# Kernel tuning notes

Hardware: AMD Instinct MI355X
Metric: run time of the kernel (lower is better)

The kernel has to match this reference:

```python
import jax, jax.numpy as jnp
import numpy as np

B, DIN, E, FACTOR, STEPS, NH = 2048, 1024, 1024, 16, 3, 8
DH = E // NH
EPS = 1e-5


def layernorm(x, g, b):
    m = x.mean(-1, keepdims=True)
    v = ((x - m) ** 2).mean(-1, keepdims=True)
    return (x - m) / jnp.sqrt(v + EPS) * g + b


def setup_inputs() -> dict:
    key = jax.random.key(0)
    ks = iter(jax.random.split(key, 32))
    r = lambda shape, s=0.02: jax.random.normal(next(ks), shape, dtype=jnp.float32) * s
    F = E * FACTOR
    return {
        "image_feat": jax.random.normal(next(ks), (B, DIN), dtype=jnp.float32),
        "text_feat": jax.random.normal(next(ks), (B, DIN), dtype=jnp.float32),
        # fusion block
        "fc1_w": r((F, DIN)), "fc1_b": jnp.zeros((F,), jnp.float32),
        "fc2_w": r((F, DIN)), "fc2_b": jnp.zeros((F,), jnp.float32),
        "fc3_w": r((E, F)), "fc3_b": jnp.zeros((E,), jnp.float32),
        "ln_g": jnp.ones((E,), jnp.float32), "ln_b": jnp.zeros((E,), jnp.float32),
        # per-step MHA + FFN + norms, stacked over STEPS
        "Wqkv": r((STEPS, 3 * E, E)), "bqkv": jnp.zeros((STEPS, 3 * E), jnp.float32),
        "Wo": r((STEPS, E, E)), "bo": jnp.zeros((STEPS, E), jnp.float32),
        "W1": r((STEPS, E, E)), "b1": jnp.zeros((STEPS, E), jnp.float32),
        "W2": r((STEPS, E, E)), "b2": jnp.zeros((STEPS, E), jnp.float32),
        "n1_g": jnp.ones((STEPS, E), jnp.float32), "n1_b": jnp.zeros((STEPS, E), jnp.float32),
        "n2_g": jnp.ones((STEPS, E), jnp.float32), "n2_b": jnp.zeros((STEPS, E), jnp.float32),
        # output projection
        "Wout": r((DIN, E)), "bout": jnp.zeros((DIN,), jnp.float32),
    }


def mha_step(q, ctx, Wqkv, bqkv, Wo, bo):
    # q: [B,E] (query len 1), ctx: [B,L,E]
    Wq, Wk, Wv = Wqkv[:E], Wqkv[E:2 * E], Wqkv[2 * E:]
    bq, bk, bv = bqkv[:E], bqkv[E:2 * E], bqkv[2 * E:]
    L = ctx.shape[1]
    qh = (q @ Wq.T + bq).reshape(B, NH, DH)
    kh = (ctx @ Wk.T + bk).reshape(B, L, NH, DH)
    vh = (ctx @ Wv.T + bv).reshape(B, L, NH, DH)
    scores = jnp.einsum("bhd,blhd->bhl", qh, kh) / jnp.sqrt(jnp.float32(DH))
    attn = jax.nn.softmax(scores, axis=-1)
    out = jnp.einsum("bhl,blhd->bhd", attn, vh).reshape(B, E)
    return out @ Wo.T + bo


def reference(image_feat, text_feat, fc1_w, fc1_b, fc2_w, fc2_b, fc3_w, fc3_b,
              ln_g, ln_b, Wqkv, bqkv, Wo, bo, W1, b1, W2, b2,
              n1_g, n1_b, n2_g, n2_b, Wout, bout):
    # fusion block (dropout = identity in eval)
    fused = (image_feat @ fc1_w.T + fc1_b) * (text_feat @ fc2_w.T + fc2_b)
    fused = layernorm(fused @ fc3_w.T + fc3_b, ln_g, ln_b)  # [B,E]
    ctx = fused[:, None, :]  # [B,1,E]
    x = fused
    for i in range(STEPS):
        attn = mha_step(x, ctx, Wqkv[i], bqkv[i], Wo[i], bo[i])
        x = x + layernorm(attn, n1_g[i], n1_b[i])
        ffn = jax.nn.relu(x @ W1[i].T + b1[i]) @ W2[i].T + b2[i]
        x = x + layernorm(ffn, n2_g[i], n2_b[i])
        ctx = jnp.concatenate([ctx, x[:, None, :]], axis=1)
    final_output = x @ Wout.T + bout  # [B,DIN]
    return final_output, ctx
```

## Files before the change

### kernel.cpp

```cpp
#include <hip/hip_runtime.h>

#define TB 256

typedef __attribute__((ext_vector_type(8))) short short8;
typedef __attribute__((ext_vector_type(4))) float f32x4;
typedef unsigned short u16;

constexpr int B_  = 2048;
constexpr int DIN = 1024;
constexpr int E   = 1024;
constexpr int F   = 16384;
constexpr int E3  = 3072;
constexpr int CH  = 4096;

struct Ptr8 { void* p[8]; };

__device__ __forceinline__ u16 f2bf(float f) {
  union { float f; unsigned u; } v; v.f = f;
  unsigned r = v.u + 0x7fffu + ((v.u >> 16) & 1u);
  return (u16)(r >> 16);
}
__device__ __forceinline__ float bf2f(u16 u) {
  union { unsigned u; float f; } v; v.u = ((unsigned)u) << 16;
  return v.f;
}

__device__ __forceinline__ void gload16(const void* g, void* l) {
  __builtin_amdgcn_global_load_lds(
      (const __attribute__((address_space(1))) void*)g,
      (__attribute__((address_space(3))) void*)l, 16, 0, 0);
}

__device__ __forceinline__ void tile_xy(int& tx, int& ty) {
  int gx = gridDim.x;
  int nwg = gx * gridDim.y;
  int wg = blockIdx.y * gx + blockIdx.x;
  if ((nwg & 7) == 0) wg = (wg & 7) * (nwg >> 3) + (wg >> 3);
  tx = wg % gx; ty = wg / gx;
}

__device__ __forceinline__ int swz16(int o) {
  return o ^ (((o >> 7) & 7) << 4);
}

__global__ __launch_bounds__(256) void cvt_kernel(const float* __restrict__ s,
                                                  u16* __restrict__ d, int n) {
  int i = (blockIdx.x * 256 + threadIdx.x) * 4;
  if (i >= n) return;
  float4 v = *(const float4*)&s[i];
  ushort4 o;
  o.x = f2bf(v.x); o.y = f2bf(v.y); o.z = f2bf(v.z); o.w = f2bf(v.w);
  *(ushort4*)&d[i] = o;
}

__global__ __launch_bounds__(256) void fill_kernel(float* p, int n, float v) {
  int i = blockIdx.x * 256 + threadIdx.x;
  if (i < n) p[i] = v;
}

__global__ __launch_bounds__(256) void relu_multi_kernel(
    Ptr8 ys, int ny, const float* __restrict__ bias, u16* __restrict__ out) {
  size_t i = ((size_t)blockIdx.x * 256 + threadIdx.x) * 4;
  int col = (int)(i & 1023);
  float4 b = *(const float4*)&bias[col];
  float a0 = b.x, a1 = b.y, a2 = b.z, a3 = b.w;
  for (int j = 0; j < ny; ++j) {
    float4 z = *(const float4*)&((const float*)ys.p[j])[i];
    a0 += z.x; a1 += z.y; a2 += z.z; a3 += z.w;
  }
  ushort4 o;
  o.x = f2bf(a0 > 0.f ? a0 : 0.f);
  o.y = f2bf(a1 > 0.f ? a1 : 0.f);
  o.z = f2bf(a2 > 0.f ? a2 : 0.f);
  o.w = f2bf(a3 > 0.f ? a3 : 0.f);
  *(ushort4*)&out[i] = o;
}

__global__ __launch_bounds__(256) void combine_out_kernel(
    Ptr8 ys, int ny, const float* __restrict__ bias, float* __restrict__ out) {
  size_t i = ((size_t)blockIdx.x * 256 + threadIdx.x) * 4;
  int col = (int)(i & 1023);
  float4 b = *(const float4*)&bias[col];
  float a0 = b.x, a1 = b.y, a2 = b.z, a3 = b.w;
  for (int j = 0; j < ny; ++j) {
    float4 z = *(const float4*)&((const float*)ys.p[j])[i];
    a0 += z.x; a1 += z.y; a2 += z.z; a3 += z.w;
  }
  out[i] = a0; out[i + 1] = a1; out[i + 2] = a2; out[i + 3] = a3;
}

template <int EPI>
__global__ __launch_bounds__(512, 2) void gemm256(
    const u16* __restrict__ A, int sA,
    const u16* __restrict__ Bw, int sB,
    const float* __restrict__ bias, const u16* __restrict__ gate,
    void* __restrict__ Out, Ptr8 pouts, int ldOut, int ksz) {
  __shared__ __align__(16) char smem[131072];
  const int tid = threadIdx.x, lane = tid & 63, w = tid >> 6;
  const int wm = w >> 2, wn = w & 3;
  int tx, ty; tile_xy(tx, ty);
  const int m0 = tx * 256, n0 = ty * 256;
  const int k0 = blockIdx.z * ksz;
  const int nt = ksz >> 6;
  const int lr = lane & 15;

  f32x4 acc[8][4] = {};

  auto stage = [&](const u16* __restrict__ G, int gs, int gr0, int kk, int tb, int j) {
    int P = j * 8192 + w * 1024 + lane * 16;
    int L = swz16(P);
    int row = L >> 7, colb = L & 127;
    gload16(G + (size_t)(gr0 + row) * gs + kk + (colb >> 1),
            &smem[tb + j * 8192 + w * 1024]);
  };
  auto rdA = [&](int tb, int mf, int kh) -> short8 {
    int Lo = (wm * 128 + mf * 16 + lr) * 128 + kh * 64 + (lane >> 4) * 16;
    return *(const short8*)&smem[tb + swz16(Lo)];
  };
  auto rdB = [&](int tb, int nf, int kh) -> short8 {
    int Lo = (wn * 64 + nf * 16 + lr) * 128 + kh * 64 + (lane >> 4) * 16;
    return *(const short8*)&smem[tb + swz16(Lo)];
  };

#pragma unroll
  for (int j = 0; j < 4; ++j) stage(A, sA, m0, k0, 0, j);
#pragma unroll
  for (int j = 0; j < 4; ++j) stage(Bw, sB, n0, k0, 65536, j);
  asm volatile("s_waitcnt vmcnt(0)" ::: "memory");
  __builtin_amdgcn_sched_barrier(0);
  __builtin_amdgcn_s_barrier();

  int cur = 0;
  for (int t = 0; t < nt; ++t) {
    const int sa = cur * 32768;
    const int sb = 65536 + cur * 32768;
    if (t + 1 < nt) {
      const int sa2 = (cur ^ 1) * 32768;
      const int sb2 = 65536 + (cur ^ 1) * 32768;
#pragma unroll
      for (int j = 0; j < 4; ++j) stage(A, sA, m0, k0 + (t + 1) * 64, sa2, j);
#pragma unroll
      for (int j = 0; j < 4; ++j) stage(Bw, sB, n0, k0 + (t + 1) * 64, sb2, j);
    }
    short8 bfr[4][2], afr[4][2];
#pragma unroll
    for (int nf = 0; nf < 4; ++nf)
#pragma unroll
      for (int kh = 0; kh < 2; ++kh) bfr[nf][kh] = rdB(sb, nf, kh);
#pragma unroll
    for (int mf = 0; mf < 4; ++mf)
#pragma unroll
      for (int kh = 0; kh < 2; ++kh) afr[mf][kh] = rdA(sa, mf, kh);
    __builtin_amdgcn_s_setprio(1);
#pragma unroll
    for (int mf = 0; mf < 4; ++mf)
#pragma unroll
      for (int nf = 0; nf < 4; ++nf)
#pragma unroll
        for (int kh = 0; kh < 2; ++kh)
          acc[mf][nf] = __builtin_amdgcn_mfma_f32_16x16x32_bf16(
              afr[mf][kh], bfr[nf][kh], acc[mf][nf], 0, 0, 0);
    __builtin_amdgcn_s_setprio(0);
#pragma unroll
    for (int mf = 0; mf < 4; ++mf)
#pragma unroll
      for (int kh = 0; kh < 2; ++kh) afr[mf][kh] = rdA(sa, 4 + mf, kh);
    __builtin_amdgcn_s_setprio(1);
#pragma unroll
    for (int mf = 0; mf < 4; ++mf)
#pragma unroll
      for (int nf = 0; nf < 4; ++nf)
#pragma unroll
        for (int kh = 0; kh < 2; ++kh)
          acc[4 + mf][nf] = __builtin_amdgcn_mfma_f32_16x16x32_bf16(
              afr[mf][kh], bfr[nf][kh], acc[4 + mf][nf], 0, 0, 0);
    __builtin_amdgcn_s_setprio(0);
    if (t + 1 < nt) {
      asm volatile("s_waitcnt vmcnt(0)" ::: "memory");
      __builtin_amdgcn_sched_barrier(0);
      __builtin_amdgcn_s_barrier();
    }
    cur ^= 1;
  }

  if (EPI == 0) {
    float* Pf = (float*)pouts.p[blockIdx.z];
    const int rb = (lane >> 4) * 4;
#pragma unroll
    for (int mf = 0; mf < 8; ++mf) {
#pragma unroll
      for (int nf = 0; nf < 4; ++nf) {
        int row0 = m0 + wm * 128 + mf * 16 + rb;
        int col  = n0 + wn * 64 + nf * 16 + lr;
#pragma unroll
        for (int r = 0; r < 4; ++r)
          Pf[(size_t)(row0 + r) * ldOut + col] = acc[mf][nf][r];
      }
    }
  } else {
    __syncthreads();
    char* wbase = smem + w * 16384;
    const int rb = (lane >> 4) * 4;
    const int g4 = lane >> 4;
#pragma unroll
    for (int mf = 0; mf < 8; ++mf) {
      char* wmf = wbase + mf * 2048;
#pragma unroll
      for (int nf = 0; nf < 4; ++nf) {
        float bv = (bias == nullptr) ? 0.f : bias[n0 + wn * 64 + nf * 16 + lr];
        int pb = nf ^ g4;
#pragma unroll
        for (int r = 0; r < 4; ++r)
          *(u16*)&wmf[(rb + r) * 128 + pb * 32 + lr * 2] =
              f2bf(acc[mf][nf][r] + bv);
      }
      asm volatile("s_waitcnt lgkmcnt(0)" ::: "memory");
      __builtin_amdgcn_sched_barrier(0);
      int rrow = lane >> 2, wb = lane & 3;
      int pb2 = wb ^ (rrow >> 2);
      short8 v0 = *(const short8*)&wmf[rrow * 128 + pb2 * 32];
      short8 v1 = *(const short8*)&wmf[rrow * 128 + pb2 * 32 + 16];
      size_t gidx = (size_t)(m0 + wm * 128 + mf * 16 + rrow) * ldOut +
                    (n0 + wn * 64 + wb * 16);
      if (EPI == 4) {
        short8 g0 = *(const short8*)&gate[gidx];
        short8 g1 = *(const short8*)&gate[gidx + 8];
        short8 o0, o1;
#pragma unroll
        for (int j = 0; j < 8; ++j) {
          o0[j] = (short)f2bf(bf2f((u16)v0[j]) * bf2f((u16)g0[j]));
          o1[j] = (short)f2bf(bf2f((u16)v1[j]) * bf2f((u16)g1[j]));
        }
        *(short8*)((u16*)Out + gidx) = o0;
        *(short8*)((u16*)Out + gidx + 8) = o1;
      } else {
        *(short8*)((u16*)Out + gidx) = v0;
        *(short8*)((u16*)Out + gidx + 8) = v1;
      }
    }
  }
}

template <int EPI>
__global__ __launch_bounds__(TB) void gemm_bt(
    const u16* __restrict__ A, int sA,
    const u16* __restrict__ Bw, int sB,
    const float* __restrict__ bias, Ptr8 outs,
    int ldOut, int Kext, int ksz) {
  __shared__ u16 As[128 * 32];
  __shared__ u16 Bs[128 * 32];
  const int tid = threadIdx.x, lane = tid & 63, w = tid >> 6;
  const int wr = w >> 1, wc = w & 1;
  int tx, ty; tile_xy(tx, ty);
  const int m0 = tx * 128, n0 = ty * 128;
  const int k0 = blockIdx.z * ksz;
  const int kend = min(k0 + ksz, Kext);

  f32x4 acc[4][4] = {};
  const int lr = lane & 15, lk = (lane >> 4) * 8;

  for (int kk = k0; kk < kend; kk += 32) {
#pragma unroll
    for (int is = 0; is < 2; ++is) {
      int c = is * 256 + tid;
      int r = c >> 2, kc = (c & 3) << 3;
      size_t lb = (size_t)(is * 256 + w * 64) * 8;
      gload16(A  + (size_t)(m0 + r) * sA + kk + kc, &As[lb]);
      gload16(Bw + (size_t)(n0 + r) * sB + kk + kc, &Bs[lb]);
    }
    __syncthreads();
    short8 af[4], bfv[4];
#pragma unroll
    for (int m = 0; m < 4; ++m)
      af[m] = *(const short8*)&As[(wr * 64 + m * 16 + lr) * 32 + lk];
#pragma unroll
    for (int n = 0; n < 4; ++n)
      bfv[n] = *(const short8*)&Bs[(wc * 64 + n * 16 + lr) * 32 + lk];
#pragma unroll
    for (int m = 0; m < 4; ++m)
#pragma unroll
      for (int n = 0; n < 4; ++n)
        acc[m][n] = __builtin_amdgcn_mfma_f32_16x16x32_bf16(af[m], bfv[n], acc[m][n], 0, 0, 0);
    __syncthreads();
  }

  float* Of = (float*)outs.p[EPI == 0 ? blockIdx.z : 0];
  const int rbase = (lane >> 4) * 4;
#pragma unroll
  for (int m = 0; m < 4; ++m) {
#pragma unroll
    for (int n = 0; n < 4; ++n) {
      int row0 = m0 + wr * 64 + m * 16 + rbase;
      int col  = n0 + wc * 64 + n * 16 + lr;
      float bv = (bias == nullptr) ? 0.f : bias[col];
#pragma unroll
      for (int r = 0; r < 4; ++r) {
        float v = acc[m][n][r] + bv;
        size_t idx = (size_t)(row0 + r) * ldOut + col;
        if (EPI == 0) Of[idx] = v;
        else          ((u16*)Of)[idx] = f2bf(v);
      }
    }
  }
}

template <int EPI>
__global__ __launch_bounds__(TB) void gemm_wf32(
    const u16* __restrict__ A, int sA,
    const float* __restrict__ Bw, int sB,
    const float* __restrict__ bias, void* __restrict__ Out, int ldOut,
    int Kext, int ksz) {
  __shared__ u16 As[128 * 32];
  __shared__ u16 Bs[128 * 32];
  const int tid = threadIdx.x, lane = tid & 63, w = tid >> 6;
  const int wr = w >> 1, wc = w & 1;
  int tx, ty; tile_xy(tx, ty);
  const int m0 = tx * 128, n0 = ty * 128;
  const int k0 = blockIdx.z * ksz;
  const int kend = min(k0 + ksz, Kext);

  f32x4 acc[4][4] = {};
  const int lr = lane & 15, lk = (lane >> 4) * 8;

  for (int kk = k0; kk < kend; kk += 32) {
#pragma unroll
    for (int is = 0; is < 2; ++is) {
      int c = is * 256 + tid;
      int r = c >> 2, kc = (c & 3) << 3;
      gload16(A + (size_t)(m0 + r) * sA + kk + kc,
              &As[(size_t)(is * 256 + w * 64) * 8]);
    }
#pragma unroll
    for (int p = 0; p < 4; ++p) {
      int t = tid + p * 256;
      int r = t >> 3, c4 = (t & 7) << 2;
      float4 v = *(const float4*)&Bw[(size_t)(n0 + r) * sB + kk + c4];
      ushort4 o;
      o.x = f2bf(v.x); o.y = f2bf(v.y); o.z = f2bf(v.z); o.w = f2bf(v.w);
      *(ushort4*)&Bs[r * 32 + c4] = o;
    }
    __syncthreads();
    short8 af[4], bfv[4];
#pragma unroll
    for (int m = 0; m < 4; ++m)
      af[m] = *(const short8*)&As[(wr * 64 + m * 16 + lr) * 32 + lk];
#pragma unroll
    for (int n = 0; n < 4; ++n)
      bfv[n] = *(const short8*)&Bs[(wc * 64 + n * 16 + lr) * 32 + lk];
#pragma unroll
    for (int m = 0; m < 4; ++m)
#pragma unroll
      for (int n = 0; n < 4; ++n)
        acc[m][n] = __builtin_amdgcn_mfma_f32_16x16x32_bf16(af[m], bfv[n], acc[m][n], 0, 0, 0);
    __syncthreads();
  }

  const int rbase = (lane >> 4) * 4;
#pragma unroll
  for (int m = 0; m < 4; ++m) {
#pragma unroll
    for (int n = 0; n < 4; ++n) {
      int row0 = m0 + wr * 64 + m * 16 + rbase;
      int col  = n0 + wc * 64 + n * 16 + lr;
      float bv = (EPI == 3 || bias == nullptr) ? 0.f : bias[col];
#pragma unroll
      for (int r = 0; r < 4; ++r) {
        float v = acc[m][n][r] + bv;
        size_t idx = (size_t)(row0 + r) * ldOut + col;
        if (EPI == 0)      ((float*)Out)[idx] = v;
        else if (EPI == 1) ((u16*)Out)[idx] = f2bf(v);
        else if (EPI == 2) ((u16*)Out)[idx] = f2bf(v > 0.f ? v : 0.f);
        else               atomicAdd((float*)Out + idx, v);
      }
    }
  }
}

__global__ __launch_bounds__(TB) void gemm_dual_wf32(
    const u16* __restrict__ A1, const u16* __restrict__ A2, int sA,
    const float* __restrict__ B1, const float* __restrict__ B2, int sB,
    const float* __restrict__ bias1, const float* __restrict__ bias2,
    u16* __restrict__ Out, int ldOut, int K) {
  __shared__ u16 As1[128 * 32];
  __shared__ u16 As2[128 * 32];
  __shared__ u16 Bs1[128 * 32];
  __shared__ u16 Bs2[128 * 32];
  const int tid = threadIdx.x, lane = tid & 63, w = tid >> 6;
  const int wr = w >> 1, wc = w & 1;
  int tx, ty; tile_xy(tx, ty);
  const int m0 = tx * 128, n0 = ty * 128;

  f32x4 acc1[4][4] = {};
  f32x4 acc2[4][4] = {};
  const int lr = lane & 15, lk = (lane >> 4) * 8;

  for (int kk = 0; kk < K; kk += 32) {
#pragma unroll
    for (int is = 0; is < 2; ++is) {
      int c = is * 256 + tid;
      int r = c >> 2, kc = (c & 3) << 3;
      size_t lb = (size_t)(is * 256 + w * 64) * 8;
      gload16(A1 + (size_t)(m0 + r) * sA + kk + kc, &As1[lb]);
      gload16(A2 + (size_t)(m0 + r) * sA + kk + kc, &As2[lb]);
    }
#pragma unroll
    for (int p = 0; p < 4; ++p) {
      int t = tid + p * 256;
      int r = t >> 3, c4 = (t & 7) << 2;
      float4 v1 = *(const float4*)&B1[(size_t)(n0 + r) * sB + kk + c4];
      float4 v2 = *(const float4*)&B2[(size_t)(n0 + r) * sB + kk + c4];
      ushort4 o1, o2;
      o1.x = f2bf(v1.x); o1.y = f2bf(v1.y); o1.z = f2bf(v1.z); o1.w = f2bf(v1.w);
      o2.x = f2bf(v2.x); o2.y = f2bf(v2.y); o2.z = f2bf(v2.z); o2.w = f2bf(v2.w);
      *(ushort4*)&Bs1[r * 32 + c4] = o1;
      *(ushort4*)&Bs2[r * 32 + c4] = o2;
    }
    __syncthreads();
    short8 a1[4], a2[4], b1v[4], b2v[4];
#pragma unroll
    for (int m = 0; m < 4; ++m) {
      a1[m] = *(const short8*)&As1[(wr * 64 + m * 16 + lr) * 32 + lk];
      a2[m] = *(const short8*)&As2[(wr * 64 + m * 16 + lr) * 32 + lk];
    }
#pragma unroll
    for (int n = 0; n < 4; ++n) {
      b1v[n] = *(const short8*)&Bs1[(wc * 64 + n * 16 + lr) * 32 + lk];
      b2v[n] = *(const short8*)&Bs2[(wc * 64 + n * 16 + lr) * 32 + lk];
    }
#pragma unroll
    for (int m = 0; m < 4; ++m)
#pragma unroll
      for (int n = 0; n < 4; ++n) {
        acc1[m][n] = __builtin_amdgcn_mfma_f32_16x16x32_bf16(a1[m], b1v[n], acc1[m][n], 0, 0, 0);
        acc2[m][n] = __builtin_amdgcn_mfma_f32_16x16x32_bf16(a2[m], b2v[n], acc2[m][n], 0, 0, 0);
      }
    __syncthreads();
  }

  const int rbase = (lane >> 4) * 4;
#pragma unroll
  for (int m = 0; m < 4; ++m) {
#pragma unroll
    for (int n = 0; n < 4; ++n) {
      int row0 = m0 + wr * 64 + m * 16 + rbase;
      int col  = n0 + wc * 64 + n * 16 + lr;
      float bv1 = bias1[col], bv2 = bias2[col];
#pragma unroll
      for (int r = 0; r < 4; ++r) {
        float v = (acc1[m][n][r] + bv1) * (acc2[m][n][r] + bv2);
        Out[(size_t)(row0 + r) * ldOut + col] = f2bf(v);
      }
    }
  }
}

template <int MODE>
__global__ __launch_bounds__(256) void resln_kernel(
    Ptr8 ys, int ny, const float* __restrict__ preb,
    const float* __restrict__ g, const float* __restrict__ bp,
    float* __restrict__ x, u16* __restrict__ xb,
    float* __restrict__ ctxo, int ctxRow) {
  const int r = blockIdx.x, tid = threadIdx.x;
  const size_t base = (size_t)r * 1024 + tid * 4;
  float y[4] = {0.f, 0.f, 0.f, 0.f};
  for (int j = 0; j < ny; ++j) {
    float4 z = *(const float4*)&((const float*)ys.p[j])[base];
    y[0] += z.x; y[1] += z.y; y[2] += z.z; y[3] += z.w;
  }
  if (preb != nullptr) {
    float4 p4 = *(const float4*)&preb[tid * 4];
    y[0] += p4.x; y[1] += p4.y; y[2] += p4.z; y[3] += p4.w;
  }
  float s = y[0] + y[1] + y[2] + y[3];
  float q = y[0] * y[0] + y[1] * y[1] + y[2] * y[2] + y[3] * y[3];
  __shared__ float red[8];
  for (int o = 32; o; o >>= 1) { s += __shfl_xor(s, o); q += __shfl_xor(q, o); }
  int wv = tid >> 6;
  if ((tid & 63) == 0) { red[wv] = s; red[4 + wv] = q; }
  __syncthreads();
  s = red[0] + red[1] + red[2] + red[3];
  q = red[4] + red[5] + red[6] + red[7];
  float mean = s * (1.f / 1024.f);
  float var  = q * (1.f / 1024.f) - mean * mean;
  float rs   = rsqrtf(var + 1e-5f);
  float4 g4 = *(const float4*)&g[tid * 4];
  float4 b4 = *(const float4*)&bp[tid * 4];
  float gg[4] = {g4.x, g4.y, g4.z, g4.w};
  float bb[4] = {b4.x, b4.y, b4.z, b4.w};
  float xv[4];
#pragma unroll
  for (int j = 0; j < 4; ++j) {
    float val = (y[j] - mean) * rs * gg[j] + bb[j];
    xv[j] = (MODE == 0) ? val : x[base + j] + val;
  }
  *(float4*)&x[base] = make_float4(xv[0], xv[1], xv[2], xv[3]);
  ushort4 xo;
  xo.x = f2bf(xv[0]); xo.y = f2bf(xv[1]); xo.z = f2bf(xv[2]); xo.w = f2bf(xv[3]);
  *(ushort4*)&xb[base] = xo;
  if (MODE != 1) {
    size_t cb = ((size_t)r * 4 + ctxRow) * 1024 + tid * 4;
    *(float4*)&ctxo[cb] = make_float4(xv[0], xv[1], xv[2], xv[3]);
  }
}

__global__ __launch_bounds__(64) void attn_kernel(
    const u16* __restrict__ q, int qstride,
    const u16* __restrict__ kv, int kvstride, int voff,
    u16* __restrict__ out, int L) {
  const int b = blockIdx.x >> 3, h = blockIdx.x & 7;
  const int lane = threadIdx.x;
  const size_t qoff = (size_t)b * qstride + h * 128;
  float q0 = bf2f(q[qoff + lane]);
  float q1 = bf2f(q[qoff + 64 + lane]);
  float sc[3];
  for (int l = 0; l < L; ++l) {
    size_t kb = ((size_t)l * B_ + b) * kvstride + h * 128;
    float p = q0 * bf2f(kv[kb + lane]) + q1 * bf2f(kv[kb + 64 + lane]);
    for (int o = 32; o; o >>= 1) p += __shfl_xor(p, o);
    sc[l] = p * 0.08838834764831843f;
  }
  float m = sc[0];
  for (int l = 1; l < L; ++l) m = fmaxf(m, sc[l]);
  float wsum = 0.f, wgt[3];
  for (int l = 0; l < L; ++l) { wgt[l] = expf(sc[l] - m); wsum += wgt[l]; }
  float inv = 1.f / wsum;
  float o0 = 0.f, o1 = 0.f;
  for (int l = 0; l < L; ++l) {
    size_t vb = ((size_t)l * B_ + b) * kvstride + voff + h * 128;
    o0 += wgt[l] * bf2f(kv[vb + lane]);
    o1 += wgt[l] * bf2f(kv[vb + 64 + lane]);
  }
  out[(size_t)b * 1024 + h * 128 + lane]      = f2bf(o0 * inv);
  out[(size_t)b * 1024 + h * 128 + 64 + lane] = f2bf(o1 * inv);
}

extern "C" void kernel_launch(void* const* d_in, const int* in_sizes, int n_in,
                              void* d_out, int out_size, void* d_ws, size_t ws_size,
                              hipStream_t stream) {
  (void)in_sizes; (void)n_in;
  const float* image = (const float*)d_in[0];
  const float* text  = (const float*)d_in[1];
  const float* fc1_w = (const float*)d_in[2];
  const float* fc1_b = (const float*)d_in[3];
  const float* fc2_w = (const float*)d_in[4];
  const float* fc2_b = (const float*)d_in[5];
  const float* fc3_w = (const float*)d_in[6];
  const float* fc3_b = (const float*)d_in[7];
  const float* ln_g  = (const float*)d_in[8];
  const float* ln_b  = (const float*)d_in[9];
  const float* Wqkv  = (const float*)d_in[10];
  const float* bqkv  = (const float*)d_in[11];
  const float* Wo    = (const float*)d_in[12];
  const float* bo    = (const float*)d_in[13];
  const float* W1    = (const float*)d_in[14];
  const float* b1    = (const float*)d_in[15];
  const float* W2    = (const float*)d_in[16];
  const float* b2    = (const float*)d_in[17];
  const float* n1_g  = (const float*)d_in[18];
  const float* n1_b  = (const float*)d_in[19];
  const float* n2_g  = (const float*)d_in[20];
  const float* n2_b  = (const float*)d_in[21];
  const float* WoutW = (const float*)d_in[22];
  const float* boutW = (const float*)d_in[23];

  float* outF   = (float*)d_out;
  float* ctxOut = outF + (size_t)B_ * DIN;
  char* ws = (char*)d_ws;

  auto cvt = [&](const float* s, u16* d, size_t n) {
    cvt_kernel<<<dim3((unsigned)((n + 1023) / 1024)), 256, 0, stream>>>(s, d, (int)n);
  };

  const size_t NEED_A = 232783872;
  if (ws_size >= NEED_A) {
    size_t off = 0;
    auto carve = [&](size_t bytes) -> char* {
      char* p = ws + off; off += (bytes + 255) & ~(size_t)255; return p;
    };
    u16* imgB  = (u16*)carve((size_t)B_ * DIN * 2);
    u16* txtB  = (u16*)carve((size_t)B_ * DIN * 2);
    u16* fc1B  = (u16*)carve((size_t)F * DIN * 2);
    u16* fc2B  = (u16*)carve((size_t)F * DIN * 2);
    u16* fc3B  = (u16*)carve((size_t)E * F * 2);
    u16* WqkvB = (u16*)carve((size_t)3 * E3 * E * 2);
    u16* WoB   = (u16*)carve((size_t)3 * E * E * 2);
    u16* W1B   = (u16*)carve((size_t)3 * E * E * 2);
    u16* W2B   = (u16*)carve((size_t)3 * E * E * 2);
    u16* WoutB = (u16*)carve((size_t)DIN * E * 2);
    char* U    = carve((size_t)B_ * F * 2);
    float* xF  = (float*)carve((size_t)B_ * E * 4);
    float* hF  = (float*)carve((size_t)B_ * E * 4);
    u16* fusedB = (u16*)U;
    u16* kvB    = (u16*)(U);
    u16* qB     = (u16*)(U + 25165824);
    u16* ctxB   = (u16*)(U + 37748736);
    u16* attnB  = (u16*)(U + 37748736 + 16777216);
    u16* h1B    = (u16*)(U + 37748736 + 16777216 + 4194304);
    u16* xbB    = (u16*)(U + 37748736 + 16777216 + 8388608);
    float* PA = (float*)fc1B;
    float* PB = (float*)(fc1B + 4194304);
    float* PC = (float*)(fc1B + 8388608);
    float* PD = (float*)(fc1B + 12582912);
    float* PE = (float*)fc2B;
    float* PF = (float*)(fc2B + 4194304);

    cvt(image, imgB, (size_t)B_ * DIN);
    cvt(text,  txtB, (size_t)B_ * DIN);
    cvt(fc1_w, fc1B, (size_t)F * DIN);
    cvt(fc2_w, fc2B, (size_t)F * DIN);
    cvt(fc3_w, fc3B, (size_t)E * F);
    cvt(Wqkv,  WqkvB, (size_t)3 * E3 * E);
    cvt(Wo,    WoB,   (size_t)3 * E * E);
    cvt(W1,    W1B,   (size_t)3 * E * E);
    cvt(W2,    W2B,   (size_t)3 * E * E);
    cvt(WoutW, WoutB, (size_t)DIN * E);

    Ptr8 dumb{};
    gemm256<1><<<dim3(B_ / 256, F / 256), 512, 0, stream>>>(
        txtB, DIN, fc2B, DIN, fc2_b, nullptr, fusedB, dumb, F, DIN);
    gemm256<4><<<dim3(B_ / 256, F / 256), 512, 0, stream>>>(
        imgB, DIN, fc1B, DIN, fc1_b, fusedB, fusedB, dumb, F, DIN);
    Ptr8 p8f{{xF, hF, PA, PB, PC, PD, PE, PF}};
    gemm256<0><<<dim3(B_ / 256, E / 256, 8), 512, 0, stream>>>(
        fusedB, F, fc3B, F, nullptr, nullptr, nullptr, p8f, E, F / 8);
    resln_kernel<0><<<B_, 256, 0, stream>>>(
        p8f, 8, fc3_b, ln_g, ln_b, xF, ctxB, ctxOut, 0);

    Ptr8 p4{{hF, outF, PA, PB, nullptr, nullptr, nullptr, nullptr}};
    for (int i = 0; i < 3; ++i) {
      int L = i + 1;
      Ptr8 qkv1{{kvB, nullptr, nullptr, nullptr, nullptr, nullptr, nullptr, nullptr}};
      gemm_bt<1><<<dim3(L * B_ / 128, 2 * E / 128), TB, 0, stream>>>(
          ctxB, E, WqkvB + (size_t)i * E3 * E + (size_t)E * E, E,
          bqkv + (size_t)i * E3 + E, qkv1, 2 * E, E, E);
      Ptr8 qkv2{{qB, nullptr, nullptr, nullptr, nullptr, nullptr, nullptr, nullptr}};
      gemm_bt<1><<<dim3(B_ / 128, E / 128), TB, 0, stream>>>(
          ctxB + (size_t)i * B_ * E, E, WqkvB + (size_t)i * E3 * E, E,
          bqkv + (size_t)i * E3, qkv2, E, E, E);
      attn_kernel<<<B_ * 8, 64, 0, stream>>>(qB, E, kvB, 2 * E, E, attnB, L);
      gemm_bt<0><<<dim3(B_ / 128, E / 128, 4), TB, 0, stream>>>(
          attnB, E, WoB + (size_t)i * E * E, E, nullptr, p4, E, E, E / 4);
      resln_kernel<1><<<B_, 256, 0, stream>>>(
          p4, 4, bo + (size_t)i * E, n1_g + (size_t)i * E, n1_b + (size_t)i * E,
          xF, xbB, nullptr, 0);
      gemm_bt<0><<<dim3(B_ / 128, E / 128, 4), TB, 0, stream>>>(
          xbB, E, W1B + (size_t)i * E * E, E, nullptr, p4, E, E, E / 4);
      relu_multi_kernel<<<B_ * E / 1024, 256, 0, stream>>>(
          p4, 4, b1 + (size_t)i * E, h1B);
      gemm_bt<0><<<dim3(B_ / 128, E / 128, 4), TB, 0, stream>>>(
          h1B, E, W2B + (size_t)i * E * E, E, nullptr, p4, E, E, E / 4);
      resln_kernel<2><<<B_, 256, 0, stream>>>(
          p4, 4, b2 + (size_t)i * E, n2_g + (size_t)i * E, n2_b + (size_t)i * E,
          xF, ctxB + (size_t)(i + 1) * B_ * E, ctxOut, i + 1);
    }

    Ptr8 pfin{{hF, PA, PB, PC, nullptr, nullptr, nullptr, nullptr}};
    gemm_bt<0><<<dim3(B_ / 128, DIN / 128, 4), TB, 0, stream>>>(
        ctxB + (size_t)3 * B_ * E, E, WoutB, E, nullptr, pfin, DIN, E, E / 4);
    combine_out_kernel<<<B_ * DIN / 1024, 256, 0, stream>>>(pfin, 4, boutW, outF);
    return;
  }

  size_t off = 0;
  auto carve = [&](size_t bytes) -> char* {
    char* p = ws + off; off += (bytes + 255) & ~(size_t)255; return p;
  };
  u16* imgB   = (u16*)carve((size_t)B_ * DIN * 2);
  u16* txtB   = (u16*)carve((size_t)B_ * DIN * 2);
  u16* fusedC = (u16*)carve((size_t)B_ * CH * 2);
  u16* qkvB   = (u16*)carve((size_t)3 * B_ * E3 * 2);
  u16* ctxB   = (u16*)carve((size_t)4 * B_ * E * 2);
  u16* attnB  = (u16*)carve((size_t)B_ * E * 2);
  u16* h1B    = (u16*)carve((size_t)B_ * E * 2);
  u16* xbB    = (u16*)carve((size_t)B_ * E * 2);
  float* xF   = (float*)carve((size_t)B_ * E * 4);
  float* hF   = (float*)carve((size_t)B_ * E * 4);

  if (off > ws_size) {
    fill_kernel<<<(out_size + 255) / 256, 256, 0, stream>>>(outF, out_size, 12345.0f);
    return;
  }

  cvt(image, imgB, (size_t)B_ * DIN);
  cvt(text,  txtB, (size_t)B_ * DIN);
  hipMemsetAsync(hF, 0, (size_t)B_ * E * 4, stream);

  for (int c = 0; c < F / CH; ++c) {
    gemm_dual_wf32<<<dim3(B_ / 128, CH / 128), TB, 0, stream>>>(
        imgB, txtB, DIN,
        fc1_w + (size_t)c * CH * DIN, fc2_w + (size_t)c * CH * DIN, DIN,
        fc1_b + (size_t)c * CH, fc2_b + (size_t)c * CH, fusedC, CH, DIN);
    gemm_wf32<3><<<dim3(B_ / 128, E / 128, 2), TB, 0, stream>>>(
        fusedC, CH, fc3_w + (size_t)c * CH, F, nullptr, hF, E, CH, CH / 2);
  }
  {
    Ptr8 y1{{hF, nullptr, nullptr, nullptr, nullptr, nullptr, nullptr, nullptr}};
    resln_kernel<0><<<B_, 256, 0, stream>>>(y1, 1, fc3_b, ln_g, ln_b, xF, ctxB, ctxOut, 0);
  }

  for (int i = 0; i < 3; ++i) {
    int L = i + 1;
    gemm_wf32<1><<<dim3(L * B_ / 128, E3 / 128), TB, 0, stream>>>(
        ctxB, E, Wqkv + (size_t)i * E3 * E, E, bqkv + (size_t)i * E3, qkvB, E3, E, E);
    attn_kernel<<<B_ * 8, 64, 0, stream>>>(
        qkvB + (size_t)(L - 1) * B_ * E3, E3, qkvB + 1024, E3, 1024, attnB, L);
    gemm_wf32<0><<<dim3(B_ / 128, E / 128), TB, 0, stream>>>(
        attnB, E, Wo + (size_t)i * E * E, E, bo + (size_t)i * E, hF, E, E, E);
    Ptr8 y1{{hF, nullptr, nullptr, nullptr, nullptr, nullptr, nullptr, nullptr}};
    resln_kernel<1><<<B_, 256, 0, stream>>>(
        y1, 1, nullptr, n1_g + (size_t)i * E, n1_b + (size_t)i * E, xF, xbB, nullptr, 0);
    gemm_wf32<2><<<dim3(B_ / 128, E / 128), TB, 0, stream>>>(
        xbB, E, W1 + (size_t)i * E * E, E, b1 + (size_t)i * E, h1B, E, E, E);
    gemm_wf32<0><<<dim3(B_ / 128, E / 128), TB, 0, stream>>>(
        h1B, E, W2 + (size_t)i * E * E, E, b2 + (size_t)i * E, hF, E, E, E);
    resln_kernel<2><<<B_, 256, 0, stream>>>(
        y1, 1, nullptr, n2_g + (size_t)i * E, n2_b + (size_t)i * E, xF,
        ctxB + (size_t)(i + 1) * B_ * E, ctxOut, i + 1);
  }
  gemm_wf32<0><<<dim3(B_ / 128, DIN / 128), TB, 0, stream>>>(
      ctxB + (size_t)3 * B_ * E, E, WoutW, E, boutW, outF, DIN, E, E);
}
```

Measured before the change: 836.6 us.

## Switch GEMM mainloop to 4-slot, 32-wide K ring with two-ahead prefetch

The 256x256 bf16 GEMM mainloop now uses K-steps of 32 instead of 64, held in a four-slot shared-memory ring, and prefetches two steps ahead. Each wait uses a partial vmcnt(4) instead of a full drain, so global loads stay in flight across iterations. Shared memory is repacked with two rows per 128-byte line to fit the shorter K slices, and a single A/B fragment set feeds all 8x4 MFMAs. The cost is twice as many barriers per K range and a different LDS bank-conflict pattern.

```diff
diff --git a/kernel.cpp b/kernel.cpp
--- a/kernel.cpp
+++ b/kernel.cpp
@@ -101,7 +101,7 @@
   int tx, ty; tile_xy(tx, ty);
   const int m0 = tx * 256, n0 = ty * 256;
   const int k0 = blockIdx.z * ksz;
-  const int nt = ksz >> 6;
+  const int nt = ksz >> 5;
   const int lr = lane & 15;
 
   f32x4 acc[8][4] = {};
@@ -109,78 +109,69 @@
   auto stage = [&](const u16* __restrict__ G, int gs, int gr0, int kk, int tb, int j) {
     int P = j * 8192 + w * 1024 + lane * 16;
     int L = swz16(P);
-    int row = L >> 7, colb = L & 127;
-    gload16(G + (size_t)(gr0 + row) * gs + kk + (colb >> 1),
-            &smem[tb + j * 8192 + w * 1024]);
+    int pr = L >> 7, sub = (L >> 6) & 1, kb = L & 63;
+    gload16(G + (size_t)(gr0 + pr * 2 + sub) * gs + kk + (kb >> 1),
+            &smem[tb + P]);
   };
-  auto rdA = [&](int tb, int mf, int kh) -> short8 {
-    int Lo = (wm * 128 + mf * 16 + lr) * 128 + kh * 64 + (lane >> 4) * 16;
-    return *(const short8*)&smem[tb + swz16(Lo)];
+  auto rdA = [&](int tb, int mf) -> short8 {
+    int r = wm * 128 + mf * 16 + lr;
+    int o = (r >> 1) * 128 + (r & 1) * 64 + (lane >> 4) * 16;
+    return *(const short8*)&smem[tb + swz16(o)];
   };
-  auto rdB = [&](int tb, int nf, int kh) -> short8 {
-    int Lo = (wn * 64 + nf * 16 + lr) * 128 + kh * 64 + (lane >> 4) * 16;
-    return *(const short8*)&smem[tb + swz16(Lo)];
+  auto rdB = [&](int tb, int nf) -> short8 {
+    int r = wn * 64 + nf * 16 + lr;
+    int o = (r >> 1) * 128 + (r & 1) * 64 + (lane >> 4) * 16;
+    return *(const short8*)&smem[tb + swz16(o)];
   };
-
-#pragma unroll
-  for (int j = 0; j < 4; ++j) stage(A, sA, m0, k0, 0, j);
-#pragma unroll
-  for (int j = 0; j < 4; ++j) stage(Bw, sB, n0, k0, 65536, j);
-  asm volatile("s_waitcnt vmcnt(0)" ::: "memory");
+  auto slotA = [](int t) { return (t & 3) * 16384; };
+  auto slotB = [](int t) { return 65536 + (t & 3) * 16384; };
+
+#pragma unroll
+  for (int j = 0; j < 2; ++j) stage(A, sA, m0, k0, slotA(0), j);
+#pragma unroll
+  for (int j = 0; j < 2; ++j) stage(Bw, sB, n0, k0, slotB(0), j);
+  if (nt > 1) {
+#pragma unroll
+    for (int j = 0; j < 2; ++j) stage(A, sA, m0, k0 + 32, slotA(1), j);
+#pragma unroll
+    for (int j = 0; j < 2; ++j) stage(Bw, sB, n0, k0 + 32, slotB(1), j);
+    asm volatile("s_waitcnt vmcnt(4)" ::: "memory");
+  } else {
+    asm volatile("s_waitcnt vmcnt(0)" ::: "memory");
+  }
   __builtin_amdgcn_sched_barrier(0);
   __builtin_amdgcn_s_barrier();
 
-  int cur = 0;
   for (int t = 0; t < nt; ++t) {
-    const int sa = cur * 32768;
-    const int sb = 65536 + cur * 32768;
+    const int sa = slotA(t), sb = slotB(t);
+    if (t + 2 < nt) {
+#pragma unroll
+      for (int j = 0; j < 2; ++j) stage(A, sA, m0, k0 + (t + 2) * 32, slotA(t + 2), j);
+#pragma unroll
+      for (int j = 0; j < 2; ++j) stage(Bw, sB, n0, k0 + (t + 2) * 32, slotB(t + 2), j);
+    }
+    short8 afr[8], bfr[4];
+#pragma unroll
+    for (int nf = 0; nf < 4; ++nf) bfr[nf] = rdB(sb, nf);
+#pragma unroll
+    for (int mf = 0; mf < 8; ++mf) afr[mf] = rdA(sa, mf);
+    __builtin_amdgcn_s_setprio(1);
+#pragma unroll
+    for (int mf = 0; mf < 8; ++mf)
+#pragma unroll
+      for (int nf = 0; nf < 4; ++nf)
+        acc[mf][nf] = __builtin_amdgcn_mfma_f32_16x16x32_bf16(
+            afr[mf], bfr[nf], acc[mf][nf], 0, 0, 0);
+    __builtin_amdgcn_s_setprio(0);
+    if (t + 2 < nt) {
+      asm volatile("s_waitcnt vmcnt(4)" ::: "memory");
+    } else if (t + 1 < nt) {
+      asm volatile("s_waitcnt vmcnt(0)" ::: "memory");
+    }
     if (t + 1 < nt) {
-      const int sa2 = (cur ^ 1) * 32768;
-      const int sb2 = 65536 + (cur ^ 1) * 32768;
-#pragma unroll
-      for (int j = 0; j < 4; ++j) stage(A, sA, m0, k0 + (t + 1) * 64, sa2, j);
-#pragma unroll
-      for (int j = 0; j < 4; ++j) stage(Bw, sB, n0, k0 + (t + 1) * 64, sb2, j);
-    }
-    short8 bfr[4][2], afr[4][2];
-#pragma unroll
-    for (int nf = 0; nf < 4; ++nf)
-#pragma unroll
-      for (int kh = 0; kh < 2; ++kh) bfr[nf][kh] = rdB(sb, nf, kh);
-#pragma unroll
-    for (int mf = 0; mf < 4; ++mf)
-#pragma unroll
-      for (int kh = 0; kh < 2; ++kh) afr[mf][kh] = rdA(sa, mf, kh);
-    __builtin_amdgcn_s_setprio(1);
-#pragma unroll
-    for (int mf = 0; mf < 4; ++mf)
-#pragma unroll
-      for (int nf = 0; nf < 4; ++nf)
-#pragma unroll
-        for (int kh = 0; kh < 2; ++kh)
-          acc[mf][nf] = __builtin_amdgcn_mfma_f32_16x16x32_bf16(
-              afr[mf][kh], bfr[nf][kh], acc[mf][nf], 0, 0, 0);
-    __builtin_amdgcn_s_setprio(0);
-#pragma unroll
-    for (int mf = 0; mf < 4; ++mf)
-#pragma unroll
-      for (int kh = 0; kh < 2; ++kh) afr[mf][kh] = rdA(sa, 4 + mf, kh);
-    __builtin_amdgcn_s_setprio(1);
-#pragma unroll
-    for (int mf = 0; mf < 4; ++mf)
-#pragma unroll
-      for (int nf = 0; nf < 4; ++nf)
-#pragma unroll
-        for (int kh = 0; kh < 2; ++kh)
-          acc[4 + mf][nf] = __builtin_amdgcn_mfma_f32_16x16x32_bf16(
-              afr[mf][kh], bfr[nf][kh], acc[4 + mf][nf], 0, 0, 0);
-    __builtin_amdgcn_s_setprio(0);
-    if (t + 1 < nt) {
-      asm volatile("s_waitcnt vmcnt(0)" ::: "memory");
       __builtin_amdgcn_sched_barrier(0);
       __builtin_amdgcn_s_barrier();
     }
-    cur ^= 1;
   }
 
   if (EPI == 0) {
```

Measured after the change: 850.7 us. Within noise of the previous version (+1.7%).
